# Optimization experiments

Hardware: AMD Instinct MI355X
Metric: run time of the kernel (lower is better)

Reference implementation:

```python
import jax, jax.numpy as jnp
import numpy as np

N = 50000      # nodes
E = 800000     # edges (avg degree 16)
IN = 64        # in_features (upper layer dim)
OUT = 32       # out_features
STEPS = 20     # n_inference_steps
LR = 0.1       # inference_lr
SLOPE = 0.2    # LeakyReLU negative slope


def setup_inputs() -> dict:
    key = jax.random.key(0)
    k1, k2, k3, k4 = jax.random.split(key, 4)
    mu_upper = jax.random.normal(k1, (N, IN), dtype=jnp.float32)
    # xavier-uniform-like scale for W [OUT, IN] and a [2*OUT]
    lim_w = float(np.sqrt(6.0 / (IN + OUT)))
    W = jax.random.uniform(k2, (OUT, IN), jnp.float32, -lim_w, lim_w)
    lim_a = float(np.sqrt(6.0 / (1 + 2 * OUT)))
    a = jax.random.uniform(k3, (2 * OUT,), jnp.float32, -lim_a, lim_a)
    edge_index = jax.random.randint(k4, (2, E), 0, N, dtype=jnp.int32)
    return {"mu_upper": mu_upper, "W": W, "a": a, "edge_index": edge_index}


def _segment_softmax(scores, dst, n_nodes):
    # numerically stable softmax grouped by destination node
    m = jax.ops.segment_max(scores, dst, num_segments=n_nodes)
    m = jnp.where(jnp.isfinite(m), m, 0.0)  # mirrors nan_to_num on -inf fill
    e = jnp.exp(scores - m[dst])
    s = jax.ops.segment_sum(e, dst, num_segments=n_nodes)
    return e / (s[dst] + 1e-8)


def reference(mu_upper, W, a, edge_index):
    src, dst = edge_index[0], edge_index[1]
    n_nodes = mu_upper.shape[0]
    out_f = W.shape[0]
    # W @ mu_upper is invariant over the inference loop
    transformed = mu_upper @ W.T                       # [N, OUT]
    a_src, a_dst = a[:out_f], a[out_f:]

    # uniform 1/degree initial attention
    deg = jax.ops.segment_sum(jnp.ones((src.shape[0],), jnp.float32), dst,
                              num_segments=n_nodes)
    alpha0 = 1.0 / (deg[dst] + 1e-8)                   # [E]
    mu0 = jnp.zeros((n_nodes, out_f), jnp.float32)

    def top_down(alpha):
        msgs = alpha[:, None] * transformed[src]       # [E, OUT]
        agg = jax.ops.segment_sum(msgs, dst, num_segments=n_nodes)
        return jax.nn.relu(agg)

    def step(carry, _):
        mu, alpha = carry
        mu_hat = top_down(alpha)
        errors = mu - mu_hat
        # a^T [err_src || err_dst] == err_src@a[:OUT] + err_dst@a[OUT:]
        scores = errors @ a_src
        scores = scores[src] + (errors @ a_dst)[dst]   # [E]
        scores = jnp.where(scores > 0, scores, SLOPE * scores)  # LeakyReLU
        alpha_new = _segment_softmax(scores, dst, n_nodes)
        mu_new = mu - LR * errors                      # inference step (no lower layer)
        return (mu_new, alpha_new), None

    (mu, alpha), _ = jax.lax.scan(step, (mu0, alpha0), None, length=STEPS)
    mu_hat = top_down(alpha)
    errors = mu - mu_hat
    return mu, errors, alpha
```

## Files before the change

### kernel.cpp

```cpp
#include <hip/hip_runtime.h>
#include <hip/hip_fp16.h>
#include <math.h>

#define N_NODES 50000
#define N_EDGES 800000
#define IN_F 64
#define OUT_F 32
#define STEPS 20
#define LR 0.1f
#define SLOPE 0.2f
#define IT_NBLK 2048
#define NODES_PER_PASS (IT_NBLK * 8)


__global__ void csr_build_pad(const int* __restrict__ src, const int* __restrict__ dst,
                              int* __restrict__ cursor, int* __restrict__ csr_pad) {
    int e = blockIdx.x * blockDim.x + threadIdx.x;
    if (e < N_EDGES) {
        int d = dst[e];
        int p = atomicAdd(&cursor[d], 1);
        csr_pad[(d << 6) + p] = src[e];
    }
}

__global__ __launch_bounds__(256) void transform_kernel(const float* __restrict__ mu_upper,
                                                        const float* __restrict__ W,
                                                        __half* __restrict__ th) {
    __shared__ float4 Ws[OUT_F][17];
    int tid = threadIdx.x;
    for (int t = tid; t < OUT_F * 16; t += 256) Ws[t >> 4][t & 15] = ((const float4*)W)[t];
    __syncthreads();
    int t = blockIdx.x * 256 + tid;
    if (t >= N_NODES * 16) return;
    int n = t >> 4, op = t & 15;
    const float4* m4 = (const float4*)(mu_upper + n * IN_F);
    float a0 = 0.f, a1 = 0.f;
#pragma unroll
    for (int k = 0; k < 16; k++) {
        float4 r = m4[k];
        float4 x = Ws[2 * op][k];
        a0 += r.x * x.x + r.y * x.y + r.z * x.z + r.w * x.w;
        float4 y = Ws[2 * op + 1][k];
        a1 += r.x * y.x + r.y * y.y + r.z * y.z + r.w * y.w;
    }
    *(__half2*)(th + n * OUT_F + 2 * op) = __floats2half2_rn(a0, a1);
}

__device__ __forceinline__ void fma_h8(uint2 u, float al, float4& agg) {
    float2 f01 = __half22float2(*(__half2*)&u.x);
    float2 f23 = __half22float2(*(__half2*)&u.y);
    agg.x = fmaf(al, f01.x, agg.x);
    agg.y = fmaf(al, f01.y, agg.y);
    agg.z = fmaf(al, f23.x, agg.z);
    agg.w = fmaf(al, f23.y, agg.w);
}


__global__ __launch_bounds__(256) void firstA_nb(
        const int* __restrict__ deg, const int* __restrict__ csr_pad,
        const __half* __restrict__ th,
        float* __restrict__ mu, const float* __restrict__ a_vec,
        float* __restrict__ s_out_src, float* __restrict__ s_out_dst) {
    int lane = threadIdx.x & 63;
    int lane32 = lane & 31;
    int po = ((threadIdx.x >> 6) << 1) + (lane >> 5);
    int eslot = lane32 >> 3, c = lane32 & 7;
    for (int nb = blockIdx.x * 8; nb < N_NODES; nb += NODES_PER_PASS) {
        int n = nb + po;
        if (n >= N_NODES) break;
        int cnt = deg[n];
        int rs = n << 6;
        int my_src = (lane32 < cnt) ? csr_pad[rs + lane32] : 0;
        float4 agg = make_float4(0.f, 0.f, 0.f, 0.f);
        int lim = cnt < 32 ? cnt : 32;
#pragma unroll
        for (int k = 0; k < 8; k++) {
            int sl = eslot + 4 * k;
            int sj = __shfl(my_src, sl, 32);
            if (sl < lim) {
                uint2 u = *(const uint2*)(th + (sj << 5) + (c << 2));
                fma_h8(u, 1.0f, agg);
            }
        }
        for (int j = rs + 32 + eslot; j < rs + cnt; j += 4) {
            uint2 u = *(const uint2*)(th + (csr_pad[j] << 5) + (c << 2));
            fma_h8(u, 1.0f, agg);
        }
#pragma unroll
        for (int off = 8; off <= 16; off <<= 1) {
            agg.x += __shfl_xor(agg.x, off, 32);
            agg.y += __shfl_xor(agg.y, off, 32);
            agg.z += __shfl_xor(agg.z, off, 32);
            agg.w += __shfl_xor(agg.w, off, 32);
        }
        if (eslot == 0) {
            float al0 = 1.0f / ((float)cnt + 1e-8f);
            float4 mh;
            mh.x = fmaxf(al0 * agg.x, 0.f);
            mh.y = fmaxf(al0 * agg.y, 0.f);
            mh.z = fmaxf(al0 * agg.z, 0.f);
            mh.w = fmaxf(al0 * agg.w, 0.f);
            float4 err = make_float4(-mh.x, -mh.y, -mh.z, -mh.w);
            float4 nm = make_float4(LR * mh.x, LR * mh.y, LR * mh.z, LR * mh.w);
            *(float4*)(mu + (n << 5) + (c << 2)) = nm;
            float4 as = *(const float4*)(a_vec + (c << 2));
            float4 ad = *(const float4*)(a_vec + OUT_F + (c << 2));
            float v1 = err.x * as.x + err.y * as.y + err.z * as.z + err.w * as.w;
            float v2 = err.x * ad.x + err.y * ad.y + err.z * ad.z + err.w * ad.w;
#pragma unroll
            for (int off = 1; off <= 4; off <<= 1) {
                v1 += __shfl_xor(v1, off, 32);
                v2 += __shfl_xor(v2, off, 32);
            }
            if (c == 0) { s_out_src[n] = v1; s_out_dst[n] = v2; }
        }
    }
}

template <bool FINAL>
__global__ __launch_bounds__(256) void fused_nb(
        const int* __restrict__ deg, const int* __restrict__ csr_pad,
        const __half* __restrict__ th,
        float* __restrict__ mu, float* __restrict__ errors_out,
        const float* __restrict__ a_vec,
        const float* __restrict__ s_in_src, const float* __restrict__ s_in_dst,
        float* __restrict__ s_out_src, float* __restrict__ s_out_dst,
        float2* __restrict__ dinv) {
    int lane = threadIdx.x & 63;
    int lane32 = lane & 31;
    int po = ((threadIdx.x >> 6) << 1) + (lane >> 5);
    int eslot = lane32 >> 3, c = lane32 & 7;
    for (int nb = blockIdx.x * 8; nb < N_NODES; nb += NODES_PER_PASS) {
        int n = nb + po;
        if (n >= N_NODES) break;
        int cnt = deg[n];
        int rs = n << 6;
        float sd = s_in_dst[n];
        int my_src = (lane32 < cnt) ? csr_pad[rs + lane32] : 0;
        float e0 = 0.f;
        if (lane32 < cnt) {
            float v = s_in_src[my_src] + sd;
            v = v > 0.f ? v : SLOPE * v;
            e0 = __expf(v);
        }
        float ssum = e0;
        for (int j2 = rs + 32 + lane32; j2 < rs + cnt; j2 += 32) {
            float v = s_in_src[csr_pad[j2]] + sd;
            v = v > 0.f ? v : SLOPE * v;
            ssum += __expf(v);
        }
#pragma unroll
        for (int off = 1; off <= 16; off <<= 1) ssum += __shfl_xor(ssum, off, 32);
        float inv = 1.0f / (ssum + 1e-8f);
        float my_alpha = e0 * inv;
        float4 agg = make_float4(0.f, 0.f, 0.f, 0.f);
        int lim = cnt < 32 ? cnt : 32;
#pragma unroll
        for (int k = 0; k < 8; k++) {
            int sl = eslot + 4 * k;
            float al = __shfl(my_alpha, sl, 32);
            int sj = __shfl(my_src, sl, 32);
            if (sl < lim) {
                uint2 u = *(const uint2*)(th + (sj << 5) + (c << 2));
                fma_h8(u, al, agg);
            }
        }
        for (int j = rs + 32 + eslot; j < rs + cnt; j += 4) {
            int sj = csr_pad[j];
            float v = s_in_src[sj] + sd;
            v = v > 0.f ? v : SLOPE * v;
            float al = __expf(v) * inv;
            uint2 u = *(const uint2*)(th + (sj << 5) + (c << 2));
            fma_h8(u, al, agg);
        }
#pragma unroll
        for (int off = 8; off <= 16; off <<= 1) {
            agg.x += __shfl_xor(agg.x, off, 32);
            agg.y += __shfl_xor(agg.y, off, 32);
            agg.z += __shfl_xor(agg.z, off, 32);
            agg.w += __shfl_xor(agg.w, off, 32);
        }
        if (eslot == 0) {
            float4* mup = (float4*)(mu + (n << 5) + (c << 2));
            float4 muv = *mup;
            float4 err;
            err.x = muv.x - fmaxf(agg.x, 0.f);
            err.y = muv.y - fmaxf(agg.y, 0.f);
            err.z = muv.z - fmaxf(agg.z, 0.f);
            err.w = muv.w - fmaxf(agg.w, 0.f);
            if (FINAL) {
                *(float4*)(errors_out + (n << 5) + (c << 2)) = err;
                if (c == 0) dinv[n] = make_float2(sd, inv);
            } else {
                float4 nm;
                nm.x = fmaf(-LR, err.x, muv.x);
                nm.y = fmaf(-LR, err.y, muv.y);
                nm.z = fmaf(-LR, err.z, muv.z);
                nm.w = fmaf(-LR, err.w, muv.w);
                *mup = nm;
                float4 as = *(const float4*)(a_vec + (c << 2));
                float4 ad = *(const float4*)(a_vec + OUT_F + (c << 2));
                float v1 = err.x * as.x + err.y * as.y + err.z * as.z + err.w * as.w;
                float v2 = err.x * ad.x + err.y * ad.y + err.z * ad.z + err.w * ad.w;
#pragma unroll
                for (int off = 1; off <= 4; off <<= 1) {
                    v1 += __shfl_xor(v1, off, 32);
                    v2 += __shfl_xor(v2, off, 32);
                }
                if (c == 0) { s_out_src[n] = v1; s_out_dst[n] = v2; }
            }
        }
    }
}

__global__ void alpha_final_kernel(const int* __restrict__ src, const int* __restrict__ dst,
                                   const float* __restrict__ s_src,
                                   const float2* __restrict__ dinv,
                                   float* __restrict__ alpha_out) {
    for (int e = blockIdx.x * blockDim.x + threadIdx.x; e < N_EDGES;
         e += IT_NBLK * 256) {
        float2 di = dinv[dst[e]];
        float v = s_src[src[e]] + di.x;
        v = v > 0.f ? v : SLOPE * v;
        alpha_out[e] = __expf(v) * di.y;
    }
}

extern "C" void kernel_launch(void* const* d_in, const int* in_sizes, int n_in,
                              void* d_out, int out_size, void* d_ws, size_t ws_size,
                              hipStream_t stream) {
    const float* mu_upper = (const float*)d_in[0];
    const float* W        = (const float*)d_in[1];
    const float* a_vec    = (const float*)d_in[2];
    const int*   edge_idx = (const int*)d_in[3];
    const int*   src = edge_idx;
    const int*   dst = edge_idx + N_EDGES;

    float* out = (float*)d_out;
    float* mu         = out;
    float* errors_out = out + N_NODES * OUT_F;
    float* alpha_out  = out + 2 * N_NODES * OUT_F;

    char* ws = (char*)d_ws;
    int*    cursor = (int*)(ws + 0);
    float*  sA     = (float*)(ws + 200064);
    float*  sB     = (float*)(ws + 400064);
    float*  sAd    = (float*)(ws + 600064);
    float*  sBd    = (float*)(ws + 800064);
    float2* dinv   = (float2*)(ws + 1000064);
    __half* th     = (__half*)(ws + 1400064);
    int*   csr_pad = (int*)(ws + 4600064);

    hipMemsetAsync(cursor, 0, N_NODES * sizeof(int), stream);

    csr_build_pad<<<(N_EDGES + 255) / 256, 256, 0, stream>>>(src, dst, cursor, csr_pad);
    transform_kernel<<<(N_NODES * 16 + 255) / 256, 256, 0, stream>>>(mu_upper, W, th);

    firstA_nb<<<IT_NBLK, 256, 0, stream>>>(cursor, csr_pad, th, mu, a_vec, sA, sAd);
    float *si = sA, *sid = sAd, *so = sB, *sod = sBd;
    for (int t = 2; t <= STEPS; t++) {
        fused_nb<false><<<IT_NBLK, 256, 0, stream>>>(cursor, csr_pad, th, mu, errors_out,
                                                     a_vec, si, sid, so, sod, dinv);
        float* tmp;
        tmp = si; si = so; so = tmp;
        tmp = sid; sid = sod; sod = tmp;
    }
    fused_nb<true><<<IT_NBLK, 256, 0, stream>>>(cursor, csr_pad, th, mu, errors_out,
                                                a_vec, si, sid, so, sod, dinv);
    alpha_final_kernel<<<IT_NBLK, 256, 0, stream>>>(src, dst, si, dinv, alpha_out);
}
```

Measured before the change: 506.9 us.

## Compress CSR indices to 16-bit, interleave score arrays, merge setup kernels

Stores padded CSR source indices as unsigned short instead of int, which halves index traffic in every iteration. The per-node source and destination scores are packed into one float2 array, and the CSR build and feature-transform kernels are merged into a single launch. The 16-bit indices rely on N=50000 fitting in 65535, and the float2 gather reads 8 bytes where only the .x half is needed for source lookups.

```diff
diff --git a/kernel.cpp b/kernel.cpp
--- a/kernel.cpp
+++ b/kernel.cpp
@@ -11,39 +11,42 @@
 #define SLOPE 0.2f
 #define IT_NBLK 2048
 #define NODES_PER_PASS (IT_NBLK * 8)
-
-
-__global__ void csr_build_pad(const int* __restrict__ src, const int* __restrict__ dst,
-                              int* __restrict__ cursor, int* __restrict__ csr_pad) {
-    int e = blockIdx.x * blockDim.x + threadIdx.x;
-    if (e < N_EDGES) {
-        int d = dst[e];
-        int p = atomicAdd(&cursor[d], 1);
-        csr_pad[(d << 6) + p] = src[e];
-    }
-}
-
-__global__ __launch_bounds__(256) void transform_kernel(const float* __restrict__ mu_upper,
-                                                        const float* __restrict__ W,
-                                                        __half* __restrict__ th) {
-    __shared__ float4 Ws[OUT_F][17];
-    int tid = threadIdx.x;
-    for (int t = tid; t < OUT_F * 16; t += 256) Ws[t >> 4][t & 15] = ((const float4*)W)[t];
-    __syncthreads();
-    int t = blockIdx.x * 256 + tid;
-    if (t >= N_NODES * 16) return;
-    int n = t >> 4, op = t & 15;
-    const float4* m4 = (const float4*)(mu_upper + n * IN_F);
-    float a0 = 0.f, a1 = 0.f;
-#pragma unroll
-    for (int k = 0; k < 16; k++) {
-        float4 r = m4[k];
-        float4 x = Ws[2 * op][k];
-        a0 += r.x * x.x + r.y * x.y + r.z * x.z + r.w * x.w;
-        float4 y = Ws[2 * op + 1][k];
-        a1 += r.x * y.x + r.y * y.y + r.z * y.z + r.w * y.w;
-    }
-    *(__half2*)(th + n * OUT_F + 2 * op) = __floats2half2_rn(a0, a1);
+#define CSR_BLKS 3125
+#define TR_BLKS 3125
+
+
+__global__ __launch_bounds__(256) void build_kernel(
+        const int* __restrict__ src, const int* __restrict__ dst,
+        int* __restrict__ cursor, unsigned short* __restrict__ csr_pad,
+        const float* __restrict__ mu_upper, const float* __restrict__ W,
+        __half* __restrict__ th) {
+    if (blockIdx.x < CSR_BLKS) {
+        int e = blockIdx.x * 256 + threadIdx.x;
+        if (e < N_EDGES) {
+            int d = dst[e];
+            int p = atomicAdd(&cursor[d], 1);
+            csr_pad[(d << 6) + p] = (unsigned short)src[e];
+        }
+    } else {
+        __shared__ float4 Ws[OUT_F][17];
+        int tid = threadIdx.x;
+        for (int t = tid; t < OUT_F * 16; t += 256) Ws[t >> 4][t & 15] = ((const float4*)W)[t];
+        __syncthreads();
+        int t = (blockIdx.x - CSR_BLKS) * 256 + tid;
+        if (t >= N_NODES * 16) return;
+        int n = t >> 4, op = t & 15;
+        const float4* m4 = (const float4*)(mu_upper + n * IN_F);
+        float a0 = 0.f, a1 = 0.f;
+#pragma unroll
+        for (int k = 0; k < 16; k++) {
+            float4 r = m4[k];
+            float4 x = Ws[2 * op][k];
+            a0 += r.x * x.x + r.y * x.y + r.z * x.z + r.w * x.w;
+            float4 y = Ws[2 * op + 1][k];
+            a1 += r.x * y.x + r.y * y.y + r.z * y.z + r.w * y.w;
+        }
+        *(__half2*)(th + n * OUT_F + 2 * op) = __floats2half2_rn(a0, a1);
+    }
 }
 
 __device__ __forceinline__ void fma_h8(uint2 u, float al, float4& agg) {
@@ -57,10 +60,10 @@
 
 
 __global__ __launch_bounds__(256) void firstA_nb(
-        const int* __restrict__ deg, const int* __restrict__ csr_pad,
+        const int* __restrict__ deg, const unsigned short* __restrict__ csr_pad,
         const __half* __restrict__ th,
         float* __restrict__ mu, const float* __restrict__ a_vec,
-        float* __restrict__ s_out_src, float* __restrict__ s_out_dst) {
+        float2* __restrict__ s_out) {
     int lane = threadIdx.x & 63;
     int lane32 = lane & 31;
     int po = ((threadIdx.x >> 6) << 1) + (lane >> 5);
@@ -70,7 +73,7 @@
         if (n >= N_NODES) break;
         int cnt = deg[n];
         int rs = n << 6;
-        int my_src = (lane32 < cnt) ? csr_pad[rs + lane32] : 0;
+        int my_src = (lane32 < cnt) ? (int)csr_pad[rs + lane32] : 0;
         float4 agg = make_float4(0.f, 0.f, 0.f, 0.f);
         int lim = cnt < 32 ? cnt : 32;
 #pragma unroll
@@ -83,7 +86,7 @@
             }
         }
         for (int j = rs + 32 + eslot; j < rs + cnt; j += 4) {
-            uint2 u = *(const uint2*)(th + (csr_pad[j] << 5) + (c << 2));
+            uint2 u = *(const uint2*)(th + ((int)csr_pad[j] << 5) + (c << 2));
             fma_h8(u, 1.0f, agg);
         }
 #pragma unroll
@@ -112,19 +115,18 @@
                 v1 += __shfl_xor(v1, off, 32);
                 v2 += __shfl_xor(v2, off, 32);
             }
-            if (c == 0) { s_out_src[n] = v1; s_out_dst[n] = v2; }
+            if (c == 0) s_out[n] = make_float2(v1, v2);
         }
     }
 }
 
 template <bool FINAL>
 __global__ __launch_bounds__(256) void fused_nb(
-        const int* __restrict__ deg, const int* __restrict__ csr_pad,
+        const int* __restrict__ deg, const unsigned short* __restrict__ csr_pad,
         const __half* __restrict__ th,
         float* __restrict__ mu, float* __restrict__ errors_out,
         const float* __restrict__ a_vec,
-        const float* __restrict__ s_in_src, const float* __restrict__ s_in_dst,
-        float* __restrict__ s_out_src, float* __restrict__ s_out_dst,
+        const float2* __restrict__ s_in, float2* __restrict__ s_out,
         float2* __restrict__ dinv) {
     int lane = threadIdx.x & 63;
     int lane32 = lane & 31;
@@ -135,17 +137,17 @@
         if (n >= N_NODES) break;
         int cnt = deg[n];
         int rs = n << 6;
-        float sd = s_in_dst[n];
-        int my_src = (lane32 < cnt) ? csr_pad[rs + lane32] : 0;
+        float sd = s_in[n].y;
+        int my_src = (lane32 < cnt) ? (int)csr_pad[rs + lane32] : 0;
         float e0 = 0.f;
         if (lane32 < cnt) {
-            float v = s_in_src[my_src] + sd;
+            float v = s_in[my_src].x + sd;
             v = v > 0.f ? v : SLOPE * v;
             e0 = __expf(v);
         }
         float ssum = e0;
         for (int j2 = rs + 32 + lane32; j2 < rs + cnt; j2 += 32) {
-            float v = s_in_src[csr_pad[j2]] + sd;
+            float v = s_in[(int)csr_pad[j2]].x + sd;
             v = v > 0.f ? v : SLOPE * v;
             ssum += __expf(v);
         }
@@ -166,8 +168,8 @@
             }
         }
         for (int j = rs + 32 + eslot; j < rs + cnt; j += 4) {
-            int sj = csr_pad[j];
-            float v = s_in_src[sj] + sd;
+            int sj = (int)csr_pad[j];
+            float v = s_in[sj].x + sd;
             v = v > 0.f ? v : SLOPE * v;
             float al = __expf(v) * inv;
             uint2 u = *(const uint2*)(th + (sj << 5) + (c << 2));
@@ -207,20 +209,20 @@
                     v1 += __shfl_xor(v1, off, 32);
                     v2 += __shfl_xor(v2, off, 32);
                 }
-                if (c == 0) { s_out_src[n] = v1; s_out_dst[n] = v2; }
+                if (c == 0) s_out[n] = make_float2(v1, v2);
             }
         }
     }
 }
 
 __global__ void alpha_final_kernel(const int* __restrict__ src, const int* __restrict__ dst,
-                                   const float* __restrict__ s_src,
+                                   const float2* __restrict__ s_fin,
                                    const float2* __restrict__ dinv,
                                    float* __restrict__ alpha_out) {
     for (int e = blockIdx.x * blockDim.x + threadIdx.x; e < N_EDGES;
          e += IT_NBLK * 256) {
         float2 di = dinv[dst[e]];
-        float v = s_src[src[e]] + di.x;
+        float v = s_fin[src[e]].x + di.x;
         v = v > 0.f ? v : SLOPE * v;
         alpha_out[e] = __expf(v) * di.y;
     }
@@ -243,29 +245,25 @@
 
     char* ws = (char*)d_ws;
     int*    cursor = (int*)(ws + 0);
-    float*  sA     = (float*)(ws + 200064);
-    float*  sB     = (float*)(ws + 400064);
-    float*  sAd    = (float*)(ws + 600064);
-    float*  sBd    = (float*)(ws + 800064);
+    float2* sA     = (float2*)(ws + 200064);
+    float2* sB     = (float2*)(ws + 600064);
     float2* dinv   = (float2*)(ws + 1000064);
     __half* th     = (__half*)(ws + 1400064);
-    int*   csr_pad = (int*)(ws + 4600064);
+    unsigned short* csr_pad = (unsigned short*)(ws + 4600064);
 
     hipMemsetAsync(cursor, 0, N_NODES * sizeof(int), stream);
 
-    csr_build_pad<<<(N_EDGES + 255) / 256, 256, 0, stream>>>(src, dst, cursor, csr_pad);
-    transform_kernel<<<(N_NODES * 16 + 255) / 256, 256, 0, stream>>>(mu_upper, W, th);
-
-    firstA_nb<<<IT_NBLK, 256, 0, stream>>>(cursor, csr_pad, th, mu, a_vec, sA, sAd);
-    float *si = sA, *sid = sAd, *so = sB, *sod = sBd;
+    build_kernel<<<CSR_BLKS + TR_BLKS, 256, 0, stream>>>(src, dst, cursor, csr_pad,
+                                                         mu_upper, W, th);
+
+    firstA_nb<<<IT_NBLK, 256, 0, stream>>>(cursor, csr_pad, th, mu, a_vec, sA);
+    float2 *si = sA, *so = sB;
     for (int t = 2; t <= STEPS; t++) {
         fused_nb<false><<<IT_NBLK, 256, 0, stream>>>(cursor, csr_pad, th, mu, errors_out,
-                                                     a_vec, si, sid, so, sod, dinv);
-        float* tmp;
-        tmp = si; si = so; so = tmp;
-        tmp = sid; sid = sod; sod = tmp;
+                                                     a_vec, si, so, dinv);
+        float2* tmp = si; si = so; so = tmp;
     }
     fused_nb<true><<<IT_NBLK, 256, 0, stream>>>(cursor, csr_pad, th, mu, errors_out,
-                                                a_vec, si, sid, so, sod, dinv);
+                                                a_vec, si, so, dinv);
     alpha_final_kernel<<<IT_NBLK, 256, 0, stream>>>(src, dst, si, dinv, alpha_out);
 }
```

Measured after the change: 512.0 us. Within noise of the previous version (+1.0%).
